# Performance work log

Measured on AMD Instinct MI355X. Metric: run time of the kernel, lower is better.

## Reference

```python
import jax, jax.numpy as jnp
import numpy as np


def _class_stats(x, labels, C):
    # x: [N, D] float scores; labels: [N] int class ids in [0, C)
    N, D = x.shape
    ones = jnp.ones((N,), x.dtype)
    counts = jax.ops.segment_sum(ones, labels, num_segments=C)                 # [C]
    sums = jax.ops.segment_sum(x, labels, num_segments=C)                      # [C, D]
    safe = jnp.maximum(counts, 1.0)
    means = sums / safe[:, None]                                               # per-class mean, [C, D]
    total = sums.sum(axis=0)                                                   # [D]
    other = (total[None, :] - sums) / jnp.maximum(N - counts, 1.0)[:, None]    # complement mean, [C, D]
    # intra-class L1 spread: mean over (count_c * D) elements per class
    intra_row = jnp.abs(x - means[labels]).sum(axis=-1)                        # [N]
    intra = jax.ops.segment_sum(intra_row, labels, num_segments=C) / (safe * D)
    diff = jnp.exp(-5.0 * jnp.abs(means - other).mean(axis=-1))                # [C]
    present = counts > 0
    n_present = present.sum()
    # original: if only one unique class, diff term is exp(0) == 1
    diff = jnp.where(n_present > 1, diff, jnp.ones_like(diff))
    return intra, diff, present


def setup_inputs() -> dict:
    key = jax.random.key(0)
    k1, k2 = jax.random.split(key)
    N, C = 2_000_000, 32
    pred = jax.random.normal(k1, (N, C), dtype=jnp.float32)
    pseudo = jax.random.normal(k2, (N, C), dtype=jnp.float32)
    return {"pred": pred, "pseudo": pseudo}


def reference(pred, pseudo):
    # used_labels=False branch of LossClassInOut
    C = pred.shape[-1]
    pseudo_labels = jnp.argmax(pseudo, axis=-1)
    pred_labels = jnp.argmax(pred, axis=-1)
    # pred stats segmented by pseudo labels; pseudo stats segmented by pred labels
    pred_loss, pred_diff, pres_a = _class_stats(pred, pseudo_labels, C)
    pseudo_loss, pseudo_diff, pres_b = _class_stats(pseudo, pred_labels, C)
    pa = pres_a.astype(pred.dtype)
    pb = pres_b.astype(pred.dtype)
    num = (pred_loss * pa).sum() + (pred_diff * pa).sum() + (pseudo_loss * pb).sum() + (pseudo_diff * pb).sum()
    den = 2.0 * pa.sum() + 2.0 * pb.sum()
    return num / den
```

## Files before the change

kernel.cpp:

```cpp
#include <hip/hip_runtime.h>


constexpr int CDIM = 32;
constexpr int NBLK = 256;
constexpr int ROWS_PER_BLOCK = 256;

typedef __attribute__((ext_vector_type(8)))  short bf16x8;
typedef __attribute__((ext_vector_type(16))) float f32x16;

__device__ __forceinline__ unsigned short f2bf(float f) {
    unsigned u = __float_as_uint(f);
    return (unsigned short)((u + 0x7FFFu + ((u >> 16) & 1u)) >> 16);
}
__device__ __forceinline__ int toff(int r, int kb) {
    return r * 32 + ((kb ^ (r & 7)) * 4);
}
__device__ __forceinline__ int argmax_row(const float4* v) {
    float b = v[0].x; int bi = 0;
#pragma unroll
    for (int k = 0; k < 8; k++) {
        int k4 = k * 4;
        if (v[k].x > b) { b = v[k].x; bi = k4; }
        if (v[k].y > b) { b = v[k].y; bi = k4 + 1; }
        if (v[k].z > b) { b = v[k].z; bi = k4 + 2; }
        if (v[k].w > b) { b = v[k].w; bi = k4 + 3; }
    }
    return bi;
}

__device__ __forceinline__ void stage_tile(const float4* __restrict__ g4,
                                           float* lds, long long wb,
                                           int nrows, int lw)
{
    const int rl = lw >> 3;
    const int kb = (lw & 7) ^ (rl & 7);
#pragma unroll
    for (int i = 0; i < 8; i++) {
        long long r = wb + 8 * i + rl; if (r >= nrows) r = nrows - 1;
        __builtin_amdgcn_global_load_lds(
            (const __attribute__((address_space(1))) void*)(g4 + r * 8 + kb),
            (__attribute__((address_space(3))) void*)(lds + i * 256),
            16, 0, 0);
    }
}

__global__ __launch_bounds__(256) void pass1_kernel(
    const float* __restrict__ pred, const float* __restrict__ pseudo,
    float* __restrict__ ws, int nrows)
{
    __shared__ __align__(16) float ptile[4][2][64 * 32];
    __shared__ __align__(16) float qtile[4][2][64 * 32];
    __shared__ __align__(16) unsigned short labs[4][64];
    __shared__ float sa[CDIM][33], sb[CDIM][33];
    __shared__ float ca[CDIM], cb[CDIM];

    const int t = threadIdx.x, wv = t >> 6, lw = t & 63;
    for (int i = t; i < CDIM * 33; i += 256) { (&sa[0][0])[i] = 0.f; (&sb[0][0])[i] = 0.f; }
    if (t < CDIM) { ca[t] = 0.f; cb[t] = 0.f; }
    __syncthreads();

    const int n = lw & 31, h = lw >> 5;

    f32x16 accP, accQ;
#pragma unroll
    for (int g = 0; g < 16; g++) { accP[g] = 0.f; accQ[g] = 0.f; }

    const float4* p4 = (const float4*)pred;
    const float4* q4 = (const float4*)pseudo;
    const long long rps = (long long)NBLK * ROWS_PER_BLOCK;
    const int nsweep = (int)((nrows + rps - 1) / rps);
    const long long wbase0 = (long long)blockIdx.x * ROWS_PER_BLOCK + wv * 64;

    stage_tile(p4, ptile[wv][0], wbase0, nrows, lw);
    stage_tile(q4, qtile[wv][0], wbase0, nrows, lw);

    for (int s = 0; s < nsweep; s++) {
        const long long wb = wbase0 + (long long)s * rps;
        const int cur = s & 1;
        if (s + 1 < nsweep) {
            const long long wb2 = wb + rps;
            stage_tile(p4, ptile[wv][cur ^ 1], wb2, nrows, lw);
            stage_tile(q4, qtile[wv][cur ^ 1], wb2, nrows, lw);
            asm volatile("s_waitcnt vmcnt(16)" ::: "memory");
        } else {
            asm volatile("s_waitcnt vmcnt(0)" ::: "memory");
        }
        __builtin_amdgcn_sched_barrier(0);
        float* pt = ptile[wv][cur];
        float* qt = qtile[wv][cur];

        const bool valid = (wb + lw) < nrows;
        int la, lbv;
        {
            float4 r_[8];
#pragma unroll
            for (int k = 0; k < 8; k++) r_[k] = *(const float4*)&qt[toff(lw, k)];
            la = argmax_row(r_);
#pragma unroll
            for (int k = 0; k < 8; k++) r_[k] = *(const float4*)&pt[toff(lw, k)];
            lbv = argmax_row(r_);
        }
        labs[wv][lw] = (unsigned short)((valid ? la : 0xFF) | ((valid ? lbv : 0xFF) << 8));
        unsafeAtomicAdd(&ca[la  & 31], valid ? 1.f : 0.f);
        unsafeAtomicAdd(&cb[lbv & 31], valid ? 1.f : 0.f);

#pragma unroll
        for (int kt = 0; kt < 4; kt++) {
            const uint4 lv = *(const uint4*)&labs[wv][kt * 16 + h * 8];
            bf16x8 aP, aQ, bP, bQ;
#pragma unroll
            for (int j = 0; j < 8; j++) {
                unsigned w32 = ((const unsigned*)&lv)[j >> 1];
                unsigned pr  = (w32 >> ((j & 1) * 16)) & 0xFFFFu;
                int laj = (int)(pr & 0xFF), lbj = (int)(pr >> 8);
                aP[j] = (short)((laj == n) ? 0x3F80 : 0);
                aQ[j] = (short)((lbj == n) ? 0x3F80 : 0);
                int r = kt * 16 + h * 8 + j;
                int o = r * 32 + (((n >> 2) ^ (r & 7)) * 4) + (n & 3);
                bP[j] = (short)f2bf(pt[o]);
                bQ[j] = (short)f2bf(qt[o]);
            }
            accP = __builtin_amdgcn_mfma_f32_32x32x16_bf16(aP, bP, accP, 0, 0, 0);
            accQ = __builtin_amdgcn_mfma_f32_32x32x16_bf16(aQ, bQ, accQ, 0, 0, 0);
        }
    }

#pragma unroll
    for (int g = 0; g < 16; g++) {
        int c = (g & 3) + 8 * (g >> 2) + 4 * h;
        unsafeAtomicAdd(&sa[c][n], accP[g]);
        unsafeAtomicAdd(&sb[c][n], accQ[g]);
    }
    __syncthreads();
    for (int i = t; i < CDIM * CDIM; i += 256) {
        int c = i >> 5, d = i & 31;
        unsafeAtomicAdd(&ws[64 + i],        sa[c][d]);
        unsafeAtomicAdd(&ws[64 + 1024 + i], sb[c][d]);
    }
    if (t < CDIM) { unsafeAtomicAdd(&ws[t], ca[t]); unsafeAtomicAdd(&ws[32 + t], cb[t]); }
}

__global__ __launch_bounds__(256) void pass2_kernel(
    const float* __restrict__ pred, const float* __restrict__ pseudo,
    float* __restrict__ ws, int nrows)
{
    __shared__ __align__(16) float ptile[4][2][64 * 32];
    __shared__ __align__(16) float qtile[4][2][64 * 32];
    __shared__ __align__(16) float mA[1024], mB[1024];
    __shared__ float ia[CDIM], ib[CDIM];

    const int t = threadIdx.x, wv = t >> 6, lw = t & 63;
    for (int i = t; i < 1024; i += 256) {
        int c = i >> 5, d = i & 31;
        int o = c * 32 + (((d >> 2) ^ (c & 7)) * 4) + (d & 3);
        mA[o] = ws[64 + i]        / fmaxf(ws[c],      1.f);
        mB[o] = ws[64 + 1024 + i] / fmaxf(ws[32 + c], 1.f);
    }
    if (t < CDIM) { ia[t] = 0.f; ib[t] = 0.f; }
    __syncthreads();

    const float4* p4 = (const float4*)pred;
    const float4* q4 = (const float4*)pseudo;
    const long long rps = (long long)NBLK * ROWS_PER_BLOCK;
    const int nsweep = (int)((nrows + rps - 1) / rps);
    const long long wbase0 = (long long)blockIdx.x * ROWS_PER_BLOCK + wv * 64;

    stage_tile(p4, ptile[wv][0], wbase0, nrows, lw);
    stage_tile(q4, qtile[wv][0], wbase0, nrows, lw);

    for (int s = 0; s < nsweep; s++) {
        const long long wb = wbase0 + (long long)s * rps;
        const int cur = s & 1;
        if (s + 1 < nsweep) {
            const long long wb2 = wb + rps;
            stage_tile(p4, ptile[wv][cur ^ 1], wb2, nrows, lw);
            stage_tile(q4, qtile[wv][cur ^ 1], wb2, nrows, lw);
            asm volatile("s_waitcnt vmcnt(16)" ::: "memory");
        } else {
            asm volatile("s_waitcnt vmcnt(0)" ::: "memory");
        }
        __builtin_amdgcn_sched_barrier(0);
        float* pt = ptile[wv][cur];
        float* qt = qtile[wv][cur];

        const bool valid = (wb + lw) < nrows;
        float4 pr[8], qr[8];
#pragma unroll
        for (int k = 0; k < 8; k++) { pr[k] = *(const float4*)&pt[toff(lw, k)];
                                      qr[k] = *(const float4*)&qt[toff(lw, k)]; }
        const int la = argmax_row(qr) & 31;
        const int lb = argmax_row(pr) & 31;
        float sA = 0.f, sB = 0.f;
#pragma unroll
        for (int k = 0; k < 8; k++) {
            float4 m4 = *(const float4*)&mA[la * 32 + ((k ^ (la & 7)) * 4)];
            sA += fabsf(pr[k].x - m4.x) + fabsf(pr[k].y - m4.y)
                + fabsf(pr[k].z - m4.z) + fabsf(pr[k].w - m4.w);
            float4 n4 = *(const float4*)&mB[lb * 32 + ((k ^ (lb & 7)) * 4)];
            sB += fabsf(qr[k].x - n4.x) + fabsf(qr[k].y - n4.y)
                + fabsf(qr[k].z - n4.z) + fabsf(qr[k].w - n4.w);
        }
        unsafeAtomicAdd(&ia[la], valid ? sA : 0.f);
        unsafeAtomicAdd(&ib[lb], valid ? sB : 0.f);
    }
    __syncthreads();
    if (t < CDIM) {
        unsafeAtomicAdd(&ws[2112 + t], ia[t]);
        unsafeAtomicAdd(&ws[2144 + t], ib[t]);
    }
}

__global__ __launch_bounds__(64) void finalize_kernel(
    const float* __restrict__ ws, float* __restrict__ out, int nrows)
{
    __shared__ float tota[CDIM];
    __shared__ float totb[CDIM];
    int t = threadIdx.x;
    if (t < CDIM) {
        float sa_ = 0.f, sb_ = 0.f;
        for (int c = 0; c < CDIM; c++) {
            sa_ += ws[64 + c * 32 + t];
            sb_ += ws[64 + 1024 + c * 32 + t];
        }
        tota[t] = sa_; totb[t] = sb_;
    }
    __syncthreads();

    const int  c   = t & 31;
    const bool isA = (t < 32);
    const float* sums = isA ? (ws + 64) : (ws + 64 + 1024);
    const float* tot  = isA ? tota : totb;
    float cnt  = isA ? ws[c]        : ws[32 + c];
    float isum = isA ? ws[2112 + c] : ws[2144 + c];

    float safe = fmaxf(cnt, 1.0f);
    float invs = 1.0f / safe;
    float invo = 1.0f / fmaxf((float)nrows - cnt, 1.0f);
    float mad = 0.f;
    for (int d = 0; d < CDIM; d++) {
        float s = sums[c * 32 + d];
        float m = s * invs;
        float o = (tot[d] - s) * invo;
        mad += fabsf(m - o);
    }
    mad *= (1.0f / CDIM);
    float diff = expf(-5.0f * mad);
    float present = (cnt > 0.f) ? 1.f : 0.f;

    unsigned long long pm = __ballot(cnt > 0.f);
    int np = isA ? __popcll(pm & 0xFFFFFFFFull) : __popcll(pm >> 32);
    if (np <= 1) diff = 1.0f;

    float intra   = isum * invs * (1.0f / CDIM);
    float contrib = present * (intra + diff);
    float pres    = present;
#pragma unroll
    for (int m = 1; m < 64; m <<= 1) {
        contrib += __shfl_xor(contrib, m, 64);
        pres    += __shfl_xor(pres,    m, 64);
    }
    if (t == 0) out[0] = contrib / (2.0f * pres);
}

extern "C" void kernel_launch(void* const* d_in, const int* in_sizes, int n_in,
                              void* d_out, int out_size, void* d_ws, size_t ws_size,
                              hipStream_t stream) {
    const float* pred   = (const float*)d_in[0];
    const float* pseudo = (const float*)d_in[1];
    float* ws  = (float*)d_ws;
    float* out = (float*)d_out;
    const int nrows = in_sizes[0] / CDIM;

    hipMemsetAsync(d_ws, 0, 2176 * sizeof(float), stream);

    dim3 grid(NBLK), block(256);
    pass1_kernel<<<grid, block, 0, stream>>>(pred, pseudo, ws, nrows);
    pass2_kernel<<<grid, block, 0, stream>>>(pred, pseudo, ws, nrows);
    finalize_kernel<<<1, 64, 0, stream>>>(ws, out, nrows);
}
```

Measured before the change: 601.9 us.

## Split each row across two half-waves and shrink per-wave tiles to 32 rows

Each wave now stages 32 rows per sweep instead of 64, with twice as many blocks. Each row's argmax and L1 distance are split across two half-waves, which exchange partial results through a cross-lane shuffle. The per-wave serial work and LDS footprint are halved, which should raise occupancy and latency hiding. In exchange there are more sweeps with smaller loads in flight, extra shuffles, and in pass 1 each half-wave now handles a single MFMA k-tile pair per iteration.

```diff
diff --git a/kernel.cpp b/kernel.cpp
--- a/kernel.cpp
+++ b/kernel.cpp
@@ -2,8 +2,8 @@
 
 
 constexpr int CDIM = 32;
-constexpr int NBLK = 256;
-constexpr int ROWS_PER_BLOCK = 256;
+constexpr int NBLK = 512;
+constexpr int ROWS_PER_BLOCK = 128;
 
 typedef __attribute__((ext_vector_type(8)))  short bf16x8;
 typedef __attribute__((ext_vector_type(16))) float f32x16;
@@ -15,17 +15,24 @@
 __device__ __forceinline__ int toff(int r, int kb) {
     return r * 32 + ((kb ^ (r & 7)) * 4);
 }
-__device__ __forceinline__ int argmax_row(const float4* v) {
-    float b = v[0].x; int bi = 0;
-#pragma unroll
-    for (int k = 0; k < 8; k++) {
+__device__ __forceinline__ void argmax16(const float4* v, float& bv, int& bi) {
+    float b = v[0].x; int i = 0;
+#pragma unroll
+    for (int k = 0; k < 4; k++) {
         int k4 = k * 4;
-        if (v[k].x > b) { b = v[k].x; bi = k4; }
-        if (v[k].y > b) { b = v[k].y; bi = k4 + 1; }
-        if (v[k].z > b) { b = v[k].z; bi = k4 + 2; }
-        if (v[k].w > b) { b = v[k].w; bi = k4 + 3; }
-    }
-    return bi;
+        if (v[k].x > b) { b = v[k].x; i = k4; }
+        if (v[k].y > b) { b = v[k].y; i = k4 + 1; }
+        if (v[k].z > b) { b = v[k].z; i = k4 + 2; }
+        if (v[k].w > b) { b = v[k].w; i = k4 + 3; }
+    }
+    bv = b; bi = i;
+}
+__device__ __forceinline__ int combine_argmax(float bv, int bc, int h2) {
+    float ov = __shfl_xor(bv, 32);
+    int   oc = __shfl_xor(bc, 32);
+    float vlo = h2 ? ov : bv, vhi = h2 ? bv : ov;
+    int   clo = h2 ? oc : bc, chi = h2 ? bc : oc;
+    return (vhi > vlo) ? chi : clo;
 }
 
 __device__ __forceinline__ void stage_tile(const float4* __restrict__ g4,
@@ -35,7 +42,7 @@
     const int rl = lw >> 3;
     const int kb = (lw & 7) ^ (rl & 7);
 #pragma unroll
-    for (int i = 0; i < 8; i++) {
+    for (int i = 0; i < 4; i++) {
         long long r = wb + 8 * i + rl; if (r >= nrows) r = nrows - 1;
         __builtin_amdgcn_global_load_lds(
             (const __attribute__((address_space(1))) void*)(g4 + r * 8 + kb),
@@ -48,9 +55,9 @@
     const float* __restrict__ pred, const float* __restrict__ pseudo,
     float* __restrict__ ws, int nrows)
 {
-    __shared__ __align__(16) float ptile[4][2][64 * 32];
-    __shared__ __align__(16) float qtile[4][2][64 * 32];
-    __shared__ __align__(16) unsigned short labs[4][64];
+    __shared__ __align__(16) float ptile[4][2][32 * 32];
+    __shared__ __align__(16) float qtile[4][2][32 * 32];
+    __shared__ __align__(16) unsigned short labs[4][32];
     __shared__ float sa[CDIM][33], sb[CDIM][33];
     __shared__ float ca[CDIM], cb[CDIM];
 
@@ -59,7 +66,7 @@
     if (t < CDIM) { ca[t] = 0.f; cb[t] = 0.f; }
     __syncthreads();
 
-    const int n = lw & 31, h = lw >> 5;
+    const int n = lw & 31, h2 = lw >> 5;
 
     f32x16 accP, accQ;
 #pragma unroll
@@ -69,7 +76,7 @@
     const float4* q4 = (const float4*)pseudo;
     const long long rps = (long long)NBLK * ROWS_PER_BLOCK;
     const int nsweep = (int)((nrows + rps - 1) / rps);
-    const long long wbase0 = (long long)blockIdx.x * ROWS_PER_BLOCK + wv * 64;
+    const long long wbase0 = (long long)blockIdx.x * ROWS_PER_BLOCK + wv * 32;
 
     stage_tile(p4, ptile[wv][0], wbase0, nrows, lw);
     stage_tile(q4, qtile[wv][0], wbase0, nrows, lw);
@@ -81,7 +88,7 @@
             const long long wb2 = wb + rps;
             stage_tile(p4, ptile[wv][cur ^ 1], wb2, nrows, lw);
             stage_tile(q4, qtile[wv][cur ^ 1], wb2, nrows, lw);
-            asm volatile("s_waitcnt vmcnt(16)" ::: "memory");
+            asm volatile("s_waitcnt vmcnt(8)" ::: "memory");
         } else {
             asm volatile("s_waitcnt vmcnt(0)" ::: "memory");
         }
@@ -89,24 +96,29 @@
         float* pt = ptile[wv][cur];
         float* qt = qtile[wv][cur];
 
-        const bool valid = (wb + lw) < nrows;
+        const int r = n;
+        const bool valid = (wb + r) < nrows;
         int la, lbv;
         {
-            float4 r_[8];
-#pragma unroll
-            for (int k = 0; k < 8; k++) r_[k] = *(const float4*)&qt[toff(lw, k)];
-            la = argmax_row(r_);
-#pragma unroll
-            for (int k = 0; k < 8; k++) r_[k] = *(const float4*)&pt[toff(lw, k)];
-            lbv = argmax_row(r_);
-        }
-        labs[wv][lw] = (unsigned short)((valid ? la : 0xFF) | ((valid ? lbv : 0xFF) << 8));
-        unsafeAtomicAdd(&ca[la  & 31], valid ? 1.f : 0.f);
-        unsafeAtomicAdd(&cb[lbv & 31], valid ? 1.f : 0.f);
-
-#pragma unroll
-        for (int kt = 0; kt < 4; kt++) {
-            const uint4 lv = *(const uint4*)&labs[wv][kt * 16 + h * 8];
+            float4 v_[4];
+#pragma unroll
+            for (int k = 0; k < 4; k++) v_[k] = *(const float4*)&qt[toff(r, 4 * h2 + k)];
+            float bv; int bi; argmax16(v_, bv, bi);
+            la = combine_argmax(bv, 16 * h2 + bi, h2);
+#pragma unroll
+            for (int k = 0; k < 4; k++) v_[k] = *(const float4*)&pt[toff(r, 4 * h2 + k)];
+            argmax16(v_, bv, bi);
+            lbv = combine_argmax(bv, 16 * h2 + bi, h2);
+        }
+        if (h2 == 0) {
+            labs[wv][r] = (unsigned short)((valid ? la : 0xFF) | ((valid ? lbv : 0xFF) << 8));
+            unsafeAtomicAdd(&ca[la & 31], valid ? 1.f : 0.f);
+            unsafeAtomicAdd(&cb[lbv & 31], valid ? 1.f : 0.f);
+        }
+
+#pragma unroll
+        for (int kt = 0; kt < 2; kt++) {
+            const uint4 lv = *(const uint4*)&labs[wv][kt * 16 + h2 * 8];
             bf16x8 aP, aQ, bP, bQ;
 #pragma unroll
             for (int j = 0; j < 8; j++) {
@@ -115,8 +127,8 @@
                 int laj = (int)(pr & 0xFF), lbj = (int)(pr >> 8);
                 aP[j] = (short)((laj == n) ? 0x3F80 : 0);
                 aQ[j] = (short)((lbj == n) ? 0x3F80 : 0);
-                int r = kt * 16 + h * 8 + j;
-                int o = r * 32 + (((n >> 2) ^ (r & 7)) * 4) + (n & 3);
+                int rr = kt * 16 + h2 * 8 + j;
+                int o = rr * 32 + (((n >> 2) ^ (rr & 7)) * 4) + (n & 3);
                 bP[j] = (short)f2bf(pt[o]);
                 bQ[j] = (short)f2bf(qt[o]);
             }
@@ -127,7 +139,7 @@
 
 #pragma unroll
     for (int g = 0; g < 16; g++) {
-        int c = (g & 3) + 8 * (g >> 2) + 4 * h;
+        int c = (g & 3) + 8 * (g >> 2) + 4 * h2;
         unsafeAtomicAdd(&sa[c][n], accP[g]);
         unsafeAtomicAdd(&sb[c][n], accQ[g]);
     }
@@ -144,8 +156,8 @@
     const float* __restrict__ pred, const float* __restrict__ pseudo,
     float* __restrict__ ws, int nrows)
 {
-    __shared__ __align__(16) float ptile[4][2][64 * 32];
-    __shared__ __align__(16) float qtile[4][2][64 * 32];
+    __shared__ __align__(16) float ptile[4][2][32 * 32];
+    __shared__ __align__(16) float qtile[4][2][32 * 32];
     __shared__ __align__(16) float mA[1024], mB[1024];
     __shared__ float ia[CDIM], ib[CDIM];
 
@@ -159,11 +171,13 @@
     if (t < CDIM) { ia[t] = 0.f; ib[t] = 0.f; }
     __syncthreads();
 
+    const int n = lw & 31, h2 = lw >> 5;
+
     const float4* p4 = (const float4*)pred;
     const float4* q4 = (const float4*)pseudo;
     const long long rps = (long long)NBLK * ROWS_PER_BLOCK;
     const int nsweep = (int)((nrows + rps - 1) / rps);
-    const long long wbase0 = (long long)blockIdx.x * ROWS_PER_BLOCK + wv * 64;
+    const long long wbase0 = (long long)blockIdx.x * ROWS_PER_BLOCK + wv * 32;
 
     stage_tile(p4, ptile[wv][0], wbase0, nrows, lw);
     stage_tile(q4, qtile[wv][0], wbase0, nrows, lw);
@@ -175,7 +189,7 @@
             const long long wb2 = wb + rps;
             stage_tile(p4, ptile[wv][cur ^ 1], wb2, nrows, lw);
             stage_tile(q4, qtile[wv][cur ^ 1], wb2, nrows, lw);
-            asm volatile("s_waitcnt vmcnt(16)" ::: "memory");
+            asm volatile("s_waitcnt vmcnt(8)" ::: "memory");
         } else {
             asm volatile("s_waitcnt vmcnt(0)" ::: "memory");
         }
@@ -183,22 +197,27 @@
         float* pt = ptile[wv][cur];
         float* qt = qtile[wv][cur];
 
-        const bool valid = (wb + lw) < nrows;
-        float4 pr[8], qr[8];
-#pragma unroll
-        for (int k = 0; k < 8; k++) { pr[k] = *(const float4*)&pt[toff(lw, k)];
-                                      qr[k] = *(const float4*)&qt[toff(lw, k)]; }
-        const int la = argmax_row(qr) & 31;
-        const int lb = argmax_row(pr) & 31;
+        const int r = n;
+        const bool valid = (wb + r) < nrows;
+        float4 pr_[4], qr_[4];
+#pragma unroll
+        for (int k = 0; k < 4; k++) { pr_[k] = *(const float4*)&pt[toff(r, 4 * h2 + k)];
+                                      qr_[k] = *(const float4*)&qt[toff(r, 4 * h2 + k)]; }
+        float bv; int bi;
+        argmax16(qr_, bv, bi);
+        const int la = combine_argmax(bv, 16 * h2 + bi, h2) & 31;
+        argmax16(pr_, bv, bi);
+        const int lb = combine_argmax(bv, 16 * h2 + bi, h2) & 31;
+
         float sA = 0.f, sB = 0.f;
 #pragma unroll
-        for (int k = 0; k < 8; k++) {
-            float4 m4 = *(const float4*)&mA[la * 32 + ((k ^ (la & 7)) * 4)];
-            sA += fabsf(pr[k].x - m4.x) + fabsf(pr[k].y - m4.y)
-                + fabsf(pr[k].z - m4.z) + fabsf(pr[k].w - m4.w);
-            float4 n4 = *(const float4*)&mB[lb * 32 + ((k ^ (lb & 7)) * 4)];
-            sB += fabsf(qr[k].x - n4.x) + fabsf(qr[k].y - n4.y)
-                + fabsf(qr[k].z - n4.z) + fabsf(qr[k].w - n4.w);
+        for (int k = 0; k < 4; k++) {
+            float4 m4 = *(const float4*)&mA[la * 32 + (((4 * h2 + k) ^ (la & 7)) * 4)];
+            sA += fabsf(pr_[k].x - m4.x) + fabsf(pr_[k].y - m4.y)
+                + fabsf(pr_[k].z - m4.z) + fabsf(pr_[k].w - m4.w);
+            float4 n4 = *(const float4*)&mB[lb * 32 + (((4 * h2 + k) ^ (lb & 7)) * 4)];
+            sB += fabsf(qr_[k].x - n4.x) + fabsf(qr_[k].y - n4.y)
+                + fabsf(qr_[k].z - n4.z) + fabsf(qr_[k].w - n4.w);
         }
         unsafeAtomicAdd(&ia[la], valid ? sA : 0.f);
         unsafeAtomicAdd(&ib[lb], valid ? sB : 0.f);
```

Result: no change. 601.0 us (-0.1%).
